# Kernel optimization log

Hardware: AMD Instinct MI355X
Metric: run time of the kernel (lower is better)

Reference implementation:

```python
import jax, jax.numpy as jnp
import numpy as np

B, T, E, H, L, V = 4, 1024, 768, 12, 6, 32000
HS = E // H
FF = 4 * E


def setup_inputs() -> dict:
    key = jax.random.key(0)
    ks = jax.random.split(key, 12)
    std = 0.02
    n = lambda k, shp: jax.random.normal(k, shp, jnp.float32) * std
    # sinusoidal position table (buffer, matches _get_pos_embed_table)
    pos = np.arange(T)[:, None].astype(np.float32)
    div = np.exp(np.arange(0, E, 2).astype(np.float32) * (-np.log(10000.0) / E))
    pet = np.zeros((T, E), np.float32)
    pet[:, 0::2] = np.sin(pos * div)
    pet[:, 1::2] = np.cos(pos * div)
    return {
        'tokens': jax.random.randint(ks[0], (B, T), 0, V),
        'targets': jax.random.randint(ks[1], (B, T), 0, V),
        'tok_emb': n(ks[2], (V, E)),
        'pet': jnp.asarray(pet),
        'wq': n(ks[3], (L, H, E, HS)),
        'wk': n(ks[4], (L, H, E, HS)),
        'wv': n(ks[5], (L, H, E, HS)),
        'w_proj': n(ks[6], (L, E, E)),
        'b_proj': jnp.zeros((L, E), jnp.float32),
        'ln1_g': jnp.ones((L, E), jnp.float32),
        'ln1_b': jnp.zeros((L, E), jnp.float32),
        'ln2_g': jnp.ones((L, E), jnp.float32),
        'ln2_b': jnp.zeros((L, E), jnp.float32),
        'w_ff1': n(ks[7], (L, E, FF)),
        'b_ff1': jnp.zeros((L, FF), jnp.float32),
        'w_ff2': n(ks[8], (L, FF, E)),
        'b_ff2': jnp.zeros((L, E), jnp.float32),
        'lnf_g': jnp.ones((E,), jnp.float32),
        'lnf_b': jnp.zeros((E,), jnp.float32),
        'w_out': n(ks[9], (E, V)),
        'b_out': jnp.zeros((V,), jnp.float32),
    }


def _ln(x, g, b, eps=1e-5):
    m = x.mean(-1, keepdims=True)
    v = ((x - m) ** 2).mean(-1, keepdims=True)
    return (x - m) / jnp.sqrt(v + eps) * g + b


def reference(tokens, targets, tok_emb, pet, wq, wk, wv, w_proj, b_proj,
              ln1_g, ln1_b, ln2_g, ln2_b, w_ff1, b_ff1, w_ff2, b_ff2,
              lnf_g, lnf_b, w_out, b_out):
    Tq = tokens.shape[1]
    x = tok_emb[tokens] + pet[:Tq]  # [B,T,E] (dropout=0 -> identity)
    mask = jnp.tril(jnp.ones((Tq, Tq), bool))
    for l in range(L):
        h = _ln(x, ln1_g[l], ln1_b[l])
        q = jnp.einsum('bte,hef->bhtf', h, wq[l])
        k = jnp.einsum('bte,hef->bhtf', h, wk[l])
        v = jnp.einsum('bte,hef->bhtf', h, wv[l])
        s = jnp.einsum('bhtf,bhsf->bhts', q, k) * (HS ** -0.5)
        s = jnp.where(mask, s, -jnp.inf)
        w = jax.nn.softmax(s, axis=-1)
        att = jnp.einsum('bhts,bhsf->bhtf', w, v)
        att = att.transpose(0, 2, 1, 3).reshape(x.shape[0], Tq, E)  # concat heads
        x = x + att @ w_proj[l] + b_proj[l]
        h2 = _ln(x, ln2_g[l], ln2_b[l])
        x = x + jax.nn.relu(h2 @ w_ff1[l] + b_ff1[l]) @ w_ff2[l] + b_ff2[l]
    x = _ln(x, lnf_g, lnf_b)
    logits = (x @ w_out + b_out).reshape(-1, V)  # [B*T, V]
    logp = jax.nn.log_softmax(logits, axis=-1)
    tgt = targets.reshape(-1)
    loss = -jnp.take_along_axis(logp, tgt[:, None], axis=1).mean()
    return logits, loss
```

## Files before the change

### kernel.cpp

```cpp
#include <hip/hip_runtime.h>
#include <math.h>

namespace {

constexpr int Bc = 4, Tc = 1024, Ec = 768, Hc = 12, Lc = 6;
constexpr int Vc = 32000, FFc = 3072, Mc = Bc * Tc;
constexpr int QKVN = 3 * Ec;

typedef __bf16 bf16x8 __attribute__((ext_vector_type(8)));
typedef float f32x4 __attribute__((ext_vector_type(4)));

__device__ __forceinline__ unsigned short f2bf(float f) {
  unsigned u = __builtin_bit_cast(unsigned, f);
  u += 0x7FFFu + ((u >> 16) & 1u);
  return (unsigned short)(u >> 16);
}

__device__ __forceinline__ float wave_sum(float v) {
#pragma unroll
  for (int off = 32; off > 0; off >>= 1) v += __shfl_xor(v, off, 64);
  return v;
}
__device__ __forceinline__ float block_sum256(float v, volatile float* red) {
  v = wave_sum(v);
  __syncthreads();
  if ((threadIdx.x & 63) == 0) red[threadIdx.x >> 6] = v;
  __syncthreads();
  return red[0] + red[1] + red[2] + red[3];
}
__device__ __forceinline__ void raw_barrier() {
  asm volatile("" ::: "memory");
  __builtin_amdgcn_s_barrier();
  asm volatile("" ::: "memory");
}

__global__ __launch_bounds__(256) void embed_k(const int* __restrict__ tokens,
                                               const float* __restrict__ emb,
                                               const float* __restrict__ pet,
                                               float* __restrict__ x) {
  int i = blockIdx.x * 256 + threadIdx.x;
  int m = i / Ec, e = i - m * Ec;
  int tok = tokens[m];
  x[i] = emb[(size_t)tok * Ec + e] + pet[(size_t)(m & (Tc - 1)) * Ec + e];
}

__global__ __launch_bounds__(256) void ln_k(const float* __restrict__ in,
                                            const float* __restrict__ g,
                                            const float* __restrict__ bb,
                                            unsigned short* __restrict__ outp) {
  __shared__ float red[4];
  int row = blockIdx.x, tid = threadIdx.x;
  const float* xr = in + (size_t)row * Ec;
  float v0 = xr[tid], v1 = xr[tid + 256], v2 = xr[tid + 512];
  float mean = block_sum256(v0 + v1 + v2, red) * (1.0f / 768.0f);
  float d0 = v0 - mean, d1 = v1 - mean, d2 = v2 - mean;
  float var = block_sum256(d0 * d0 + d1 * d1 + d2 * d2, red) * (1.0f / 768.0f);
  float rs = rsqrtf(var + 1e-5f);
  unsigned short* orow = outp + (size_t)row * Ec;
  orow[tid]       = f2bf(d0 * rs * g[tid]       + bb[tid]);
  orow[tid + 256] = f2bf(d1 * rs * g[tid + 256] + bb[tid + 256]);
  orow[tid + 512] = f2bf(d2 * rs * g[tid + 512] + bb[tid + 512]);
}

__global__ __launch_bounds__(256) void tcvt_k(const float* __restrict__ src,
                                              unsigned short* __restrict__ dst,
                                              int K, int N,
                                              size_t srcBatch, size_t dstBatch) {
  __shared__ float t[64][65];
  const float* s = src + blockIdx.z * srcBatch;
  unsigned short* d = dst + blockIdx.z * dstBatch;
  int k0 = blockIdx.y * 64, n0 = blockIdx.x * 64;
  int tid = threadIdx.x;
#pragma unroll
  for (int i = 0; i < 16; ++i) {
    int rr = (tid >> 6) + i * 4, cc = tid & 63;
    t[rr][cc] = s[(size_t)(k0 + rr) * N + n0 + cc];
  }
  __syncthreads();
#pragma unroll
  for (int i = 0; i < 16; ++i) {
    int rr = (tid >> 6) + i * 4, cc = tid & 63;
    d[(size_t)(n0 + rr) * K + k0 + cc] = f2bf(t[cc][rr]);
  }
}

__global__ __launch_bounds__(256) void qcvt_k(const float* __restrict__ wq,
                                              const float* __restrict__ wk,
                                              const float* __restrict__ wv,
                                              unsigned short* __restrict__ dst) {
  __shared__ float t[64][65];
  const int which = blockIdx.y / (Lc * Hc);
  const int z = blockIdx.y % (Lc * Hc), l = z / Hc, h = z % Hc;
  const float* src = which == 0 ? wq : (which == 1 ? wk : wv);
  const int k0 = blockIdx.x * 64;
  const int tid = threadIdx.x;
  const float* s = src + ((size_t)z * Ec + k0) * 64;
  unsigned short* d =
      dst + (size_t)l * QKVN * Ec + ((size_t)which * Ec + h * 64) * Ec + k0;
#pragma unroll
  for (int i = 0; i < 16; ++i) {
    int rr = (tid >> 6) + i * 4, cc = tid & 63;
    t[rr][cc] = s[(size_t)rr * 64 + cc];
  }
  __syncthreads();
#pragma unroll
  for (int i = 0; i < 16; ++i) {
    int rr = (tid >> 6) + i * 4, cc = tid & 63;
    d[(size_t)rr * Ec + cc] = f2bf(t[cc][rr]);
  }
}

#define GLDS16(g, l)                                              \
  __builtin_amdgcn_global_load_lds(                               \
      (const __attribute__((address_space(1))) void*)(g),         \
      (__attribute__((address_space(3))) void*)(l), 16, 0, 0)

template <int MODE, int BSRC, int BM, int BN, int GX>
__global__ __launch_bounds__(256) void mgemm_k(
    const unsigned short* __restrict__ A, const void* __restrict__ Bv,
    const float* __restrict__ bias, void* __restrict__ Cv,
    int M, int N, int K) {
  constexpr int MI = BM / 32, NF = BN / 32;
  constexpr int TL = BM / 32 + BN / 32;
  __shared__ unsigned short AsU[2][BM * 64];
  __shared__ unsigned short BsU[2][BN * 64];
  const int tid = threadIdx.x, lane = tid & 63, wave = tid >> 6;
  int bm, bn;
  if constexpr (GX == 1) {
    bm = blockIdx.y * BM;
    bn = blockIdx.x * BN;
  } else {
    bm = (blockIdx.z * GX + blockIdx.x) * BM;
    bn = blockIdx.y * BN;
  }
  const int wm = (wave >> 1) * (BM / 2), wn = (wave & 1) * (BN / 2);
  const int fr = lane & 15, fq = lane >> 4;
  const int lr8 = lane >> 3, lc8 = (lane & 7) * 8;
  const int sc8 = ((lane & 7) ^ (lr8 & 7)) * 8;
  f32x4 acc[MI][NF];
#pragma unroll
  for (int i = 0; i < MI; ++i)
#pragma unroll
    for (int j = 0; j < NF; ++j) acc[i][j] = (f32x4){0.f, 0.f, 0.f, 0.f};

  auto stage = [&](int k0, int pb) {
    {
      const unsigned short* g =
          A + (size_t)(bm + wave * (BM / 4) + lr8) * K + k0 + sc8;
      unsigned short* l = &AsU[pb][(wave * (BM / 4) + lr8) * 64 + lc8];
#pragma unroll
      for (int it = 0; it < BM / 32; ++it)
        GLDS16(g + (size_t)(it * 8) * K, l + it * 8 * 64);
    }
    if constexpr (BSRC == 0) {
      const unsigned short* Bt = (const unsigned short*)Bv;
      const unsigned short* g =
          Bt + (size_t)(bn + wave * (BN / 4) + lr8) * K + k0 + sc8;
      unsigned short* l = &BsU[pb][(wave * (BN / 4) + lr8) * 64 + lc8];
#pragma unroll
      for (int it = 0; it < BN / 32; ++it)
        GLDS16(g + (size_t)(it * 8) * K, l + it * 8 * 64);
    } else {
      const float* Bf = (const float*)Bv;
#pragma unroll
      for (int i = 0; i < 8; ++i) {
        int f4 = i * 256 + tid;
        int kk = f4 >> 5, c4 = (f4 & 31) * 4;
        float4 v = *(const float4*)(Bf + (size_t)(k0 + kk) * N + bn + c4);
        BsU[pb][(c4 + 0) * 64 + kk] = f2bf(v.x);
        BsU[pb][(c4 + 1) * 64 + kk] = f2bf(v.y);
        BsU[pb][(c4 + 2) * 64 + kk] = f2bf(v.z);
        BsU[pb][(c4 + 3) * 64 + kk] = f2bf(v.w);
      }
    }
  };

  auto compute = [&](int pb) {
#pragma unroll
    for (int kk = 0; kk < 2; ++kk) {
      bf16x8 af[MI], bfr[NF];
#pragma unroll
      for (int i = 0; i < MI; ++i) {
        int row = wm + i * 16 + fr;
        af[i] = *(const bf16x8*)((char*)AsU[pb] + row * 128 +
                                 ((kk * 64 + fq * 16) ^ ((row & 7) << 4)));
      }
#pragma unroll
      for (int j = 0; j < NF; ++j) {
        int row = wn + j * 16 + fr;
        if constexpr (BSRC == 0)
          bfr[j] = *(const bf16x8*)((char*)BsU[pb] + row * 128 +
                                    ((kk * 64 + fq * 16) ^ ((row & 7) << 4)));
        else
          bfr[j] = *(const bf16x8*)&BsU[pb][row * 64 + kk * 32 + fq * 8];
      }
#pragma unroll
      for (int i = 0; i < MI; ++i)
#pragma unroll
        for (int j = 0; j < NF; ++j)
          acc[i][j] = __builtin_amdgcn_mfma_f32_16x16x32_bf16(af[i], bfr[j],
                                                              acc[i][j], 0, 0, 0);
    }
  };

  const int nk = K >> 6;
  if constexpr (BSRC == 0) {
    stage(0, 0);
    for (int t = 0; t < nk; ++t) {
      const int pb = t & 1;
      if (t + 1 < nk) {
        stage((t + 1) << 6, pb ^ 1);
        if constexpr (TL == 8)      asm volatile("s_waitcnt vmcnt(8)" ::: "memory");
        else if constexpr (TL == 6) asm volatile("s_waitcnt vmcnt(6)" ::: "memory");
        else                        asm volatile("s_waitcnt vmcnt(4)" ::: "memory");
      } else {
        asm volatile("s_waitcnt vmcnt(0)" ::: "memory");
      }
      raw_barrier();
      compute(pb);
      raw_barrier();
    }
  } else {
    stage(0, 0);
    __syncthreads();
    for (int t = 0; t < nk; ++t) {
      const int pb = t & 1;
      if (t + 1 < nk) stage((t + 1) << 6, pb ^ 1);
      compute(pb);
      __syncthreads();
    }
  }
#pragma unroll
  for (int i = 0; i < MI; ++i) {
    int row0 = bm + wm + i * 16 + fq * 4;
#pragma unroll
    for (int j = 0; j < NF; ++j) {
      int col = bn + wn + j * 16 + fr;
      float bval = 0.f;
      if constexpr (MODE != 0) bval = bias[col];
#pragma unroll
      for (int r = 0; r < 4; ++r) {
        size_t idx = (size_t)(row0 + r) * N + col;
        float v = acc[i][j][r];
        if constexpr (MODE == 0) {
          ((unsigned short*)Cv)[idx] = f2bf(v);
        } else if constexpr (MODE == 1) {
          ((unsigned short*)Cv)[idx] = f2bf(fmaxf(v + bval, 0.f));
        } else if constexpr (MODE == 2) {
          float* C = (float*)Cv;
          C[idx] = C[idx] + v + bval;
        } else {
          ((float*)Cv)[idx] = v + bval;
        }
      }
    }
  }
}

template <int MI2>
__global__ __launch_bounds__(256) void fattn2_k(const unsigned short* __restrict__ qkv,
                                                unsigned short* __restrict__ att) {
  __shared__ unsigned short Ks[2][64 * 64];
  __shared__ unsigned short Vt[2][80 * 64];
  __shared__ unsigned short Pb[4][16 * 72];
  const int bh = blockIdx.y;
  const int b = bh / Hc, h = bh % Hc;
  const int qb = gridDim.x - 1 - blockIdx.x;
  const int q0 = qb * (64 * MI2);
  const int tid = threadIdx.x, lane = tid & 63, w = tid >> 6;
  const int fr = lane & 15, fq = lane >> 4;
  const size_t base = (size_t)b * Tc * QKVN + h * 64;
  const int r0 = tid >> 3, c0 = (tid & 7) * 8;
  const int s2 = (tid & 31) * 2, c0v = (tid >> 5) * 8;
  const float SC = 0.125f * 1.44269504f;

  bf16x8 aq[MI2][2];
#pragma unroll
  for (int mi = 0; mi < MI2; ++mi) {
    const unsigned short* qp =
        qkv + base + (size_t)(q0 + w * 16 * MI2 + mi * 16 + fr) * QKVN + fq * 8;
    aq[mi][0] = *(const bf16x8*)qp;
    aq[mi][1] = *(const bf16x8*)(qp + 32);
  }
  f32x4 o[MI2][5];
  float m_run[MI2][4];
#pragma unroll
  for (int mi = 0; mi < MI2; ++mi)
#pragma unroll
    for (int n = 0; n < 5; ++n) o[mi][n] = (f32x4){0.f, 0.f, 0.f, 0.f};
#pragma unroll
  for (int mi = 0; mi < MI2; ++mi)
#pragma unroll
    for (int r = 0; r < 4; ++r) m_run[mi][r] = -INFINITY;

  {
#pragma unroll
    for (int bx = 0; bx < 2; ++bx) {
      unsigned* vt32 = (unsigned*)(Vt[bx] + 64 * 64);
      vt32[tid] = (tid < 32) ? 0x3F803F80u : 0u;
      vt32[tid + 256] = 0u;
    }
  }

  const int nt = MI2 * (qb + 1);
  uint4 pk0, pk1, pv0, pv1;
  auto loadt = [&](int s0) {
    const unsigned short* kg = qkv + base + Ec + (size_t)(s0 + r0) * QKVN + c0;
    pk0 = *(const uint4*)kg;
    pk1 = *(const uint4*)(kg + (size_t)32 * QKVN);
    const unsigned short* vg =
        qkv + base + 2 * Ec + (size_t)(s0 + s2) * QKVN + c0v;
    pv0 = *(const uint4*)vg;
    pv1 = *(const uint4*)(vg + QKVN);
  };
  auto writet = [&](int bx) {
    *(uint4*)((char*)Ks[bx] + (r0 * 128 + ((c0 * 2) ^ ((r0 & 7) << 4)))) = pk0;
    const int r1 = r0 + 32;
    *(uint4*)((char*)Ks[bx] + (r1 * 128 + ((c0 * 2) ^ ((r1 & 7) << 4)))) = pk1;
    const unsigned short* p0 = (const unsigned short*)&pv0;
    const unsigned short* p1 = (const unsigned short*)&pv1;
#pragma unroll
    for (int j = 0; j < 8; ++j) {
      int hs = c0v + j;
      unsigned pk = (unsigned)p0[j] | ((unsigned)p1[j] << 16);
      *(unsigned*)((char*)Vt[bx] + (hs * 128 + ((s2 * 2) ^ ((hs & 7) << 4)))) = pk;
    }
  };

  loadt(0);
  writet(0);
  __syncthreads();

  for (int it = 0; it < nt; ++it) {
    const int s0 = it * 64;
    const int pb = it & 1;
    if (it + 1 < nt) loadt(s0 + 64);

    f32x4 s[MI2][4];
#pragma unroll
    for (int mi = 0; mi < MI2; ++mi)
#pragma unroll
      for (int n = 0; n < 4; ++n) s[mi][n] = (f32x4){0.f, 0.f, 0.f, 0.f};
    __builtin_amdgcn_s_setprio(1);
#pragma unroll
    for (int ss = 0; ss < 2; ++ss)
#pragma unroll
      for (int n = 0; n < 4; ++n) {
        int row = n * 16 + fr;
        bf16x8 kb = *(const bf16x8*)(
            (char*)Ks[pb] + (row * 128 + ((ss * 64 + fq * 16) ^ ((row & 7) << 4))));
#pragma unroll
        for (int mi = 0; mi < MI2; ++mi)
          s[mi][n] = __builtin_amdgcn_mfma_f32_16x16x32_bf16(aq[mi][ss], kb,
                                                             s[mi][n], 0, 0, 0);
      }
    __builtin_amdgcn_s_setprio(0);

#pragma unroll
    for (int mi = 0; mi < MI2; ++mi) {
      const int qlo = q0 + w * 16 * MI2 + mi * 16;
      const bool need_mask = (s0 + 63 > qlo);
#pragma unroll
      for (int n = 0; n < 4; ++n) {
        int scol = s0 + n * 16 + fr;
#pragma unroll
        for (int r = 0; r < 4; ++r) {
          float v = s[mi][n][r] * SC;
          if (need_mask && scol > qlo + fq * 4 + r) v = -INFINITY;
          s[mi][n][r] = v;
        }
      }
      bool ok = true;
#pragma unroll
      for (int n = 0; n < 4; ++n)
#pragma unroll
        for (int r = 0; r < 4; ++r)
          ok &= (s[mi][n][r] <= m_run[mi][r] + 8.f);
      if (!__all(ok)) {
        float mt[4];
#pragma unroll
        for (int r = 0; r < 4; ++r)
          mt[r] = fmaxf(fmaxf(s[mi][0][r], s[mi][1][r]),
                        fmaxf(s[mi][2][r], s[mi][3][r]));
#pragma unroll
        for (int off = 1; off <= 8; off <<= 1)
#pragma unroll
          for (int r = 0; r < 4; ++r)
            mt[r] = fmaxf(mt[r], __shfl_xor(mt[r], off, 64));
        float alpha[4];
#pragma unroll
        for (int r = 0; r < 4; ++r) {
          float mn = fmaxf(m_run[mi][r], mt[r]);
          alpha[r] = exp2f(m_run[mi][r] - mn);
          m_run[mi][r] = mn;
        }
#pragma unroll
        for (int n = 0; n < 5; ++n)
#pragma unroll
          for (int r = 0; r < 4; ++r) o[mi][n][r] *= alpha[r];
      }
#pragma unroll
      for (int n = 0; n < 4; ++n)
#pragma unroll
        for (int r = 0; r < 4; ++r)
          Pb[w][(fq * 4 + r) * 72 + n * 16 + fr] =
              f2bf(exp2f(s[mi][n][r] - m_run[mi][r]));
      __builtin_amdgcn_s_setprio(1);
#pragma unroll
      for (int ss = 0; ss < 2; ++ss) {
        bf16x8 pa = *(const bf16x8*)&Pb[w][fr * 72 + ss * 32 + fq * 8];
#pragma unroll
        for (int n = 0; n < 5; ++n) {
          int row = n * 16 + fr;
          bf16x8 vb = *(const bf16x8*)(
              (char*)Vt[pb] + (row * 128 + ((ss * 64 + fq * 16) ^ ((row & 7) << 4))));
          o[mi][n] = __builtin_amdgcn_mfma_f32_16x16x32_bf16(pa, vb, o[mi][n],
                                                             0, 0, 0);
        }
      }
      __builtin_amdgcn_s_setprio(0);
    }

    if (it + 1 < nt) writet(pb ^ 1);
    __syncthreads();
  }
#pragma unroll
  for (int mi = 0; mi < MI2; ++mi)
#pragma unroll
    for (int r = 0; r < 4; ++r) {
      const float l = __shfl(o[mi][4][r], lane & 48, 64);
      const float inv = 1.0f / l;
      const int qrow = q0 + w * 16 * MI2 + mi * 16 + fq * 4 + r;
      unsigned short* orow = att + ((size_t)(b * Tc + qrow)) * Ec + h * 64;
#pragma unroll
      for (int n = 0; n < 4; ++n) orow[n * 16 + fr] = f2bf(o[mi][n][r] * inv);
    }
}

__global__ __launch_bounds__(256) void loss_k(const float* __restrict__ logits,
                                              const int* __restrict__ targets,
                                              float* __restrict__ rowloss) {
  __shared__ float redm[4], reds[4];
  const int row = blockIdx.x, tid = threadIdx.x;
  const f32x4* lr4 = (const f32x4*)(logits + (size_t)row * Vc);
  float m = -INFINITY, s = 0.f;
  for (int j = tid; j < Vc / 4; j += 256) {
    f32x4 v = __builtin_nontemporal_load(lr4 + j);
    float m0 = fmaxf(fmaxf(v[0], v[1]), fmaxf(v[2], v[3]));
    float nm = fmaxf(m, m0);
    s = s * __expf(m - nm) + __expf(v[0] - nm) + __expf(v[1] - nm) +
        __expf(v[2] - nm) + __expf(v[3] - nm);
    m = nm;
  }
#pragma unroll
  for (int off = 32; off; off >>= 1) {
    float om = __shfl_xor(m, off, 64), os = __shfl_xor(s, off, 64);
    float nm = fmaxf(m, om);
    s = s * __expf(m - nm) + os * __expf(om - nm);
    m = nm;
  }
  if ((tid & 63) == 0) { redm[tid >> 6] = m; reds[tid >> 6] = s; }
  __syncthreads();
  if (tid == 0) {
    float M2 = redm[0], S2 = reds[0];
#pragma unroll
    for (int w = 1; w < 4; ++w) {
      float om = redm[w], os = reds[w];
      float nm = fmaxf(M2, om);
      S2 = S2 * __expf(M2 - nm) + os * __expf(om - nm);
      M2 = nm;
    }
    float lt = logits[(size_t)row * Vc + targets[row]];
    rowloss[row] = -(lt - M2 - logf(S2));
  }
}

__global__ __launch_bounds__(1024) void lossred_k(const float* __restrict__ rowloss,
                                                  float* __restrict__ outp) {
  __shared__ float red[16];
  float s = 0.f;
  for (int i = threadIdx.x; i < Mc; i += 1024) s += rowloss[i];
  s = wave_sum(s);
  if ((threadIdx.x & 63) == 0) red[threadIdx.x >> 6] = s;
  __syncthreads();
  if (threadIdx.x == 0) {
    float tot = 0.f;
#pragma unroll
    for (int i = 0; i < 16; ++i) tot += red[i];
    outp[0] = tot * (1.0f / (float)Mc);
  }
}

}

extern "C" void kernel_launch(void* const* d_in, const int* in_sizes, int n_in,
                              void* d_out, int out_size, void* d_ws, size_t ws_size,
                              hipStream_t stream) {
  const int*   tokens  = (const int*)d_in[0];
  const int*   targets = (const int*)d_in[1];
  const float* tok_emb = (const float*)d_in[2];
  const float* pet     = (const float*)d_in[3];
  const float* wq      = (const float*)d_in[4];
  const float* wk      = (const float*)d_in[5];
  const float* wv      = (const float*)d_in[6];
  const float* w_proj  = (const float*)d_in[7];
  const float* b_proj  = (const float*)d_in[8];
  const float* ln1_g   = (const float*)d_in[9];
  const float* ln1_b   = (const float*)d_in[10];
  const float* ln2_g   = (const float*)d_in[11];
  const float* ln2_b   = (const float*)d_in[12];
  const float* w_ff1   = (const float*)d_in[13];
  const float* b_ff1   = (const float*)d_in[14];
  const float* w_ff2   = (const float*)d_in[15];
  const float* b_ff2   = (const float*)d_in[16];
  const float* lnf_g   = (const float*)d_in[17];
  const float* lnf_b   = (const float*)d_in[18];
  const float* w_out   = (const float*)d_in[19];
  const float* b_out   = (const float*)d_in[20];

  float* out = (float*)d_out;
  char* ob = (char*)d_out;
  unsigned short* qkvA  = (unsigned short*)(ob + 0);
  unsigned short* attA  = (unsigned short*)(ob + 18874368);
  unsigned short* ffhA  = (unsigned short*)(ob + 25165824);
  unsigned short* qkvT  = (unsigned short*)(ob + 50331648);
  unsigned short* projT = (unsigned short*)(ob + 71565312);
  unsigned short* ff1T  = (unsigned short*)(ob + 78643200);
  unsigned short* ff2T  = (unsigned short*)(ob + 106954752);
  char* wb = (char*)d_ws;
  float* x = (float*)wb;
  unsigned short* hbuf = (unsigned short*)(wb + 12582912);
  float* rowloss = (float*)(wb + 18874368);
  unsigned short* woutT = (unsigned short*)(wb + 18890752);
  const bool wfit = ws_size >= (size_t)18890752 + 49152000;

  qcvt_k<<<dim3(12, 3 * Lc * Hc), 256, 0, stream>>>(wq, wk, wv, qkvT);
  tcvt_k<<<dim3(12, 12, 6), 256, 0, stream>>>(w_proj, projT, 768, 768,
                                              (size_t)589824, (size_t)589824);
  tcvt_k<<<dim3(48, 12, 6), 256, 0, stream>>>(w_ff1, ff1T, 768, 3072,
                                              (size_t)768 * 3072, (size_t)768 * 3072);
  tcvt_k<<<dim3(12, 48, 6), 256, 0, stream>>>(w_ff2, ff2T, 3072, 768,
                                              (size_t)768 * 3072, (size_t)768 * 3072);
  if (wfit)
    tcvt_k<<<dim3(500, 12, 1), 256, 0, stream>>>(w_out, woutT, 768, 32000, 0, 0);

  embed_k<<<(Mc * Ec) / 256, 256, 0, stream>>>(tokens, tok_emb, pet, x);

  for (int l = 0; l < Lc; ++l) {
    ln_k<<<Mc, 256, 0, stream>>>(x, ln1_g + (size_t)l * Ec, ln1_b + (size_t)l * Ec, hbuf);
    mgemm_k<0, 0, 128, 64, 1><<<dim3(36, 32), 256, 0, stream>>>(
        hbuf, qkvT + (size_t)l * QKVN * Ec, nullptr, qkvA, Mc, QKVN, Ec);
    fattn2_k<1><<<dim3(Tc / 64, Bc * Hc), 256, 0, stream>>>(qkvA, attA);
    mgemm_k<2, 0, 64, 64, 1><<<dim3(12, 64), 256, 0, stream>>>(
        attA, projT + (size_t)l * Ec * Ec, b_proj + (size_t)l * Ec, x, Mc, Ec, Ec);
    ln_k<<<Mc, 256, 0, stream>>>(x, ln2_g + (size_t)l * Ec, ln2_b + (size_t)l * Ec, hbuf);
    mgemm_k<1, 0, 128, 64, 1><<<dim3(48, 32), 256, 0, stream>>>(
        hbuf, ff1T + (size_t)l * Ec * FFc, b_ff1 + (size_t)l * FFc, ffhA, Mc, FFc, Ec);
    mgemm_k<2, 0, 64, 64, 1><<<dim3(12, 64), 256, 0, stream>>>(
        ffhA, ff2T + (size_t)l * Ec * FFc, b_ff2 + (size_t)l * Ec, x, Mc, Ec, FFc);
  }
  ln_k<<<Mc, 256, 0, stream>>>(x, lnf_g, lnf_b, hbuf);
  if (wfit)
    mgemm_k<3, 0, 128, 128, 32><<<dim3(32, 250, 1), 256, 0, stream>>>(
        hbuf, woutT, b_out, out, Mc, Vc, Ec);
  else
    mgemm_k<3, 1, 128, 128, 1><<<dim3(250, 32), 256, 0, stream>>>(
        hbuf, w_out, b_out, out, Mc, Vc, Ec);
  loss_k<<<Mc, 256, 0, stream>>>(out, targets, rowloss);
  lossred_k<<<1, 1024, 0, stream>>>(rowloss, out + (size_t)Mc * Vc);
}
```

Baseline: 1.589 ms.

## Fuse log-softmax partial sums into LM-head GEMM epilogue

After: 1.535 ms, median of 2. -3.4%, faster.

```diff
diff --git a/kernel.cpp b/kernel.cpp
--- a/kernel.cpp
+++ b/kernel.cpp
@@ -119,7 +119,7 @@
 __global__ __launch_bounds__(256) void mgemm_k(
     const unsigned short* __restrict__ A, const void* __restrict__ Bv,
     const float* __restrict__ bias, void* __restrict__ Cv,
-    int M, int N, int K) {
+    int M, int N, int K, float* __restrict__ pbuf) {
   constexpr int MI = BM / 32, NF = BN / 32;
   constexpr int TL = BM / 32 + BN / 32;
   __shared__ unsigned short AsU[2][BM * 64];
@@ -229,6 +229,46 @@
       compute(pb);
       __syncthreads();
     }
+  }
+  if constexpr (MODE == 4) {
+    float* pms = (float*)AsU;
+    float* C = (float*)Cv;
+    float srow[MI][4];
+#pragma unroll
+    for (int i = 0; i < MI; ++i) {
+      int row0 = bm + wm + i * 16 + fq * 4;
+#pragma unroll
+      for (int r = 0; r < 4; ++r) {
+        float s = 0.f;
+#pragma unroll
+        for (int j = 0; j < NF; ++j) {
+          int col = bn + wn + j * 16 + fr;
+          float v = acc[i][j][r] + bias[col];
+          C[(size_t)(row0 + r) * N + col] = v;
+          s += __expf(v);
+        }
+        srow[i][r] = s;
+      }
+    }
+#pragma unroll
+    for (int off = 1; off <= 8; off <<= 1)
+#pragma unroll
+      for (int i = 0; i < MI; ++i)
+#pragma unroll
+        for (int r = 0; r < 4; ++r)
+          srow[i][r] += __shfl_xor(srow[i][r], off, 64);
+    if (fr == 0) {
+#pragma unroll
+      for (int i = 0; i < MI; ++i)
+#pragma unroll
+        for (int r = 0; r < 4; ++r)
+          pms[(wm + i * 16 + fq * 4 + r) * 2 + (wave & 1)] = srow[i][r];
+    }
+    __syncthreads();
+    if (tid < BM)
+      pbuf[(size_t)(bm + tid) * 250 + (bn >> 7)] =
+          pms[tid * 2 + 0] + pms[tid * 2 + 1];
+    return;
   }
 #pragma unroll
   for (int i = 0; i < MI; ++i) {
@@ -435,6 +475,22 @@
 #pragma unroll
       for (int n = 0; n < 4; ++n) orow[n * 16 + fr] = f2bf(o[mi][n][r] * inv);
     }
+}
+
+__global__ __launch_bounds__(256) void lossfin_k(const float* __restrict__ pbuf,
+                                                 const float* __restrict__ logits,
+                                                 const int* __restrict__ targets,
+                                                 float* __restrict__ rowloss) {
+  const int row = blockIdx.x * 4 + (threadIdx.x >> 6);
+  const int lane = threadIdx.x & 63;
+  const float* p = pbuf + (size_t)row * 250;
+  float s = 0.f;
+  for (int j = lane; j < 250; j += 64) s += p[j];
+  s = wave_sum(s);
+  if (lane == 0) {
+    float lt = logits[(size_t)row * Vc + targets[row]];
+    rowloss[row] = logf(s) - lt;
+  }
 }
 
 __global__ __launch_bounds__(256) void loss_k(const float* __restrict__ logits,
@@ -532,7 +588,9 @@
   unsigned short* hbuf = (unsigned short*)(wb + 12582912);
   float* rowloss = (float*)(wb + 18874368);
   unsigned short* woutT = (unsigned short*)(wb + 18890752);
+  float* pbuf = (float*)(wb + 68042752);
   const bool wfit = ws_size >= (size_t)18890752 + 49152000;
+  const bool pfit = ws_size >= (size_t)68042752 + 4096000;
 
   qcvt_k<<<dim3(12, 3 * Lc * Hc), 256, 0, stream>>>(wq, wk, wv, qkvT);
   tcvt_k<<<dim3(12, 12, 6), 256, 0, stream>>>(w_proj, projT, 768, 768,
@@ -549,23 +607,29 @@
   for (int l = 0; l < Lc; ++l) {
     ln_k<<<Mc, 256, 0, stream>>>(x, ln1_g + (size_t)l * Ec, ln1_b + (size_t)l * Ec, hbuf);
     mgemm_k<0, 0, 128, 64, 1><<<dim3(36, 32), 256, 0, stream>>>(
-        hbuf, qkvT + (size_t)l * QKVN * Ec, nullptr, qkvA, Mc, QKVN, Ec);
+        hbuf, qkvT + (size_t)l * QKVN * Ec, nullptr, qkvA, Mc, QKVN, Ec, nullptr);
     fattn2_k<1><<<dim3(Tc / 64, Bc * Hc), 256, 0, stream>>>(qkvA, attA);
     mgemm_k<2, 0, 64, 64, 1><<<dim3(12, 64), 256, 0, stream>>>(
-        attA, projT + (size_t)l * Ec * Ec, b_proj + (size_t)l * Ec, x, Mc, Ec, Ec);
+        attA, projT + (size_t)l * Ec * Ec, b_proj + (size_t)l * Ec, x, Mc, Ec, Ec, nullptr);
     ln_k<<<Mc, 256, 0, stream>>>(x, ln2_g + (size_t)l * Ec, ln2_b + (size_t)l * Ec, hbuf);
     mgemm_k<1, 0, 128, 64, 1><<<dim3(48, 32), 256, 0, stream>>>(
-        hbuf, ff1T + (size_t)l * Ec * FFc, b_ff1 + (size_t)l * FFc, ffhA, Mc, FFc, Ec);
+        hbuf, ff1T + (size_t)l * Ec * FFc, b_ff1 + (size_t)l * FFc, ffhA, Mc, FFc, Ec, nullptr);
     mgemm_k<2, 0, 64, 64, 1><<<dim3(12, 64), 256, 0, stream>>>(
-        ffhA, ff2T + (size_t)l * Ec * FFc, b_ff2 + (size_t)l * Ec, x, Mc, Ec, FFc);
+        ffhA, ff2T + (size_t)l * Ec * FFc, b_ff2 + (size_t)l * Ec, x, Mc, Ec, FFc, nullptr);
   }
   ln_k<<<Mc, 256, 0, stream>>>(x, lnf_g, lnf_b, hbuf);
-  if (wfit)
+  if (wfit && pfit) {
+    mgemm_k<4, 0, 128, 128, 32><<<dim3(32, 250, 1), 256, 0, stream>>>(
+        hbuf, woutT, b_out, out, Mc, Vc, Ec, pbuf);
+    lossfin_k<<<Mc / 4, 256, 0, stream>>>(pbuf, out, targets, rowloss);
+  } else if (wfit) {
     mgemm_k<3, 0, 128, 128, 32><<<dim3(32, 250, 1), 256, 0, stream>>>(
-        hbuf, woutT, b_out, out, Mc, Vc, Ec);
-  else
+        hbuf, woutT, b_out, out, Mc, Vc, Ec, nullptr);
+    loss_k<<<Mc, 256, 0, stream>>>(out, targets, rowloss);
+  } else {
     mgemm_k<3, 1, 128, 128, 1><<<dim3(250, 32), 256, 0, stream>>>(
-        hbuf, w_out, b_out, out, Mc, Vc, Ec);
-  loss_k<<<Mc, 256, 0, stream>>>(out, targets, rowloss);
+        hbuf, w_out, b_out, out, Mc, Vc, Ec, nullptr);
+    loss_k<<<Mc, 256, 0, stream>>>(out, targets, rowloss);
+  }
   lossred_k<<<1, 1024, 0, stream>>>(rowloss, out + (size_t)Mc * Vc);
 }
```
